# Optimization experiments

Hardware: AMD Instinct MI355X
Metric: run time of the kernel (lower is better)

Reference implementation:

```python
import jax, jax.numpy as jnp
import numpy as np

N = 262144        # total nodes in the batched graph
E = 8388608       # edges (avg degree 32)
DIM = 128         # gin_dimension
MAXDEG = 64       # max_node_deg + 1 (embedding table rows)
BN_EPS = 1e-5
SLOPE = 0.01      # leaky_relu default negative slope


def _batchnorm(x, gamma, beta):
    # training-mode BatchNorm1d: batch statistics over the node dimension
    mu = x.mean(axis=0)
    var = x.var(axis=0)
    return (x - mu) / jnp.sqrt(var + BN_EPS) * gamma + beta


def setup_inputs() -> dict:
    key = jax.random.key(0)
    ks = jax.random.split(key, 12)
    node_deg = jax.random.randint(ks[0], (N,), 0, MAXDEG)
    edge_index = jax.random.randint(ks[1], (2, E), 0, N)
    pos = jax.random.normal(ks[2], (N, 3), dtype=jnp.float32)
    # learned parameters
    embed_deg = jax.random.normal(ks[3], (MAXDEG, DIM), dtype=jnp.float32) * 0.02
    eps = jnp.zeros((), dtype=jnp.float32)  # GINConv train_eps, init 0
    W_conv = jax.random.normal(ks[4], (3, DIM), dtype=jnp.float32) * 0.5
    b_conv = jnp.full((DIM,), 0.01, dtype=jnp.float32)
    bn1_gamma = jnp.ones((DIM,), dtype=jnp.float32)
    bn1_beta = jnp.zeros((DIM,), dtype=jnp.float32)
    fc_W1 = jax.random.normal(ks[5], (2 * DIM, DIM), dtype=jnp.float32) * 0.06
    fc_b1 = jnp.full((DIM,), 0.01, dtype=jnp.float32)
    fc_bn_gamma = jnp.ones((DIM,), dtype=jnp.float32)
    fc_bn_beta = jnp.zeros((DIM,), dtype=jnp.float32)
    fc_W2 = jax.random.normal(ks[6], (DIM, 1), dtype=jnp.float32) * 0.12
    fc_b2 = jnp.full((1,), 0.01, dtype=jnp.float32)
    return {
        "node_deg": node_deg, "edge_index": edge_index, "pos": pos,
        "embed_deg": embed_deg, "eps": eps, "W_conv": W_conv, "b_conv": b_conv,
        "bn1_gamma": bn1_gamma, "bn1_beta": bn1_beta,
        "fc_W1": fc_W1, "fc_b1": fc_b1,
        "fc_bn_gamma": fc_bn_gamma, "fc_bn_beta": fc_bn_beta,
        "fc_W2": fc_W2, "fc_b2": fc_b2,
    }


def reference(node_deg, edge_index, pos, embed_deg, eps, W_conv, b_conv,
              bn1_gamma, bn1_beta, fc_W1, fc_b1, fc_bn_gamma, fc_bn_beta,
              fc_W2, fc_b2):
    src, dst = edge_index[0], edge_index[1]
    # GINConv (train_eps): mlp((1+eps)*x + sum_{j->i} x_j), mlp = Linear(3, DIM)
    agg = jax.ops.segment_sum(pos[src], dst, num_segments=N)  # [N, 3]
    x = ((1.0 + eps) * pos + agg) @ W_conv + b_conv            # [N, DIM]
    x = jax.nn.leaky_relu(_batchnorm(x, bn1_gamma, bn1_beta), SLOPE)
    # degree embedding branch
    tmp = embed_deg[node_deg]                                  # [N, DIM]
    xc = jnp.concatenate([tmp, x], axis=1)                     # [N, 2*DIM]
    # fc head: Linear -> BN -> LeakyReLU -> Linear -> Sigmoid -> squeeze
    h = xc @ fc_W1 + fc_b1
    h = jax.nn.leaky_relu(_batchnorm(h, fc_bn_gamma, fc_bn_beta), SLOPE)
    out = jax.nn.sigmoid(h @ fc_W2 + fc_b2)
    return out[:, 0]                                           # [N] node filtration values
```

## Files before the change

kernel.cpp:

```cpp
#include <hip/hip_runtime.h>

#define N_NODES 262144
#define N_EDGES 8388608
#define EPB 8192
#define NBLK (N_EDGES / EPB)
#define NBKT 1024

typedef unsigned int uint32;
typedef unsigned short ushort16;
typedef __attribute__((ext_vector_type(8))) short short8v;
typedef __attribute__((ext_vector_type(4))) float f32x4;

__device__ __forceinline__ float bf2f(uint32 u) { return __uint_as_float(u << 16); }
__device__ __forceinline__ ushort16 f2bf(float x) {
    uint32 u = __float_as_uint(x);
    u = (u + 0x7fffu + ((u >> 16) & 1u)) >> 16;
    return (ushort16)u;
}
__device__ __forceinline__ float lrelu(float v) { return v > 0.f ? v : 0.01f * v; }

__global__ __launch_bounds__(256) void k_hist(const int* __restrict__ ei,
                                              uint32* __restrict__ counts) {
    __shared__ uint32 cnt[NBKT];
    int t = threadIdx.x;
    for (int j = t; j < NBKT; j += 256) cnt[j] = 0;
    __syncthreads();
    int base = blockIdx.x * EPB;
    for (int ch = 0; ch < EPB / 256; ++ch) {
        int d = ei[N_EDGES + base + ch * 256 + t];
        atomicAdd(&cnt[d >> 8], 1u);
    }
    __syncthreads();
    for (int j = t; j < NBKT; j += 256) counts[blockIdx.x * NBKT + j] = cnt[j];
}

__global__ __launch_bounds__(256) void k_scanB(const uint32* __restrict__ counts,
                                               uint32* __restrict__ offsL,
                                               uint32* __restrict__ btot) {
    int b = blockIdx.x, t = threadIdx.x;
    uint32 a[4], s = 0;
    #pragma unroll
    for (int j = 0; j < 4; ++j) { a[j] = counts[(4 * t + j) * NBKT + b]; s += a[j]; }
    int lane = t & 63, wid = t >> 6;
    uint32 v = s;
    #pragma unroll
    for (int o = 1; o < 64; o <<= 1) {
        uint32 u = __shfl_up(v, o, 64);
        if (lane >= o) v += u;
    }
    __shared__ uint32 wt[4];
    if (lane == 63) wt[wid] = v;
    __syncthreads();
    uint32 wbase = 0;
    for (int w = 0; w < wid; ++w) wbase += wt[w];
    uint32 run = wbase + v - s;
    #pragma unroll
    for (int j = 0; j < 4; ++j) { offsL[(4 * t + j) * NBKT + b] = run; run += a[j]; }
    if (t == 255) btot[b] = run;
}

__global__ __launch_bounds__(256) void k_scanTot(const uint32* __restrict__ btot,
                                                 uint32* __restrict__ bstart) {
    int t = threadIdx.x;
    uint32 c[4], s = 0;
    #pragma unroll
    for (int j = 0; j < 4; ++j) { c[j] = btot[t * 4 + j]; s += c[j]; }
    int lane = t & 63, wid = t >> 6;
    uint32 v = s;
    #pragma unroll
    for (int o = 1; o < 64; o <<= 1) {
        uint32 u = __shfl_up(v, o, 64);
        if (lane >= o) v += u;
    }
    __shared__ uint32 wt[4];
    if (lane == 63) wt[wid] = v;
    __syncthreads();
    uint32 wbase = 0;
    for (int w = 0; w < wid; ++w) wbase += wt[w];
    uint32 run = wbase + v - s;
    #pragma unroll
    for (int j = 0; j < 4; ++j) { bstart[t * 4 + j] = run; run += c[j]; }
}

__global__ __launch_bounds__(256) void k_bin(const int* __restrict__ ei,
                                             const uint32* __restrict__ offsL,
                                             const uint32* __restrict__ bstart,
                                             uint32* __restrict__ binned) {
    __shared__ uint32 cnt[NBKT];
    __shared__ uint32 base[NBKT];
    int t = threadIdx.x;
    for (int j = t; j < NBKT; j += 256) {
        cnt[j] = 0;
        base[j] = bstart[j] + offsL[blockIdx.x * NBKT + j];
    }
    __syncthreads();
    int eb = blockIdx.x * EPB;
    for (int ch = 0; ch < EPB / 256; ++ch) {
        int e = eb + ch * 256 + t;
        uint32 s = (uint32)ei[e];
        uint32 d = (uint32)ei[N_EDGES + e];
        uint32 b = d >> 8;
        uint32 r = atomicAdd(&cnt[b], 1u);
        binned[base[b] + r] = (s << 8) | (d & 255u);
    }
}

__global__ __launch_bounds__(256) void k_accum(const uint32* __restrict__ binned,
                                               const uint32* __restrict__ bstart,
                                               const uint32* __restrict__ btot,
                                               const float* __restrict__ pos,
                                               float* __restrict__ agg) {
    __shared__ float acc[768];
    int t = threadIdx.x;
    acc[t] = 0.f; acc[256 + t] = 0.f; acc[512 + t] = 0.f;
    __syncthreads();
    int b = blockIdx.x;
    uint32 st = bstart[b], ct = btot[b];
    for (uint32 i = t; i < ct; i += 256) {
        uint32 w = binned[st + i];
        uint32 s = w >> 8, dl = w & 255u;
        const float* p = pos + 3 * s;
        float p0 = p[0], p1 = p[1], p2 = p[2];
        atomicAdd(&acc[dl * 3 + 0], p0);
        atomicAdd(&acc[dl * 3 + 1], p1);
        atomicAdd(&acc[dl * 3 + 2], p2);
    }
    __syncthreads();
    float* o = agg + (size_t)b * 768;
    o[t] = acc[t]; o[256 + t] = acc[256 + t]; o[512 + t] = acc[512 + t];
}

__global__ __launch_bounds__(256) void k_scatter(const int* __restrict__ ei,
                                                 const float* __restrict__ pos,
                                                 float* __restrict__ agg) {
    int e = blockIdx.x * 256 + threadIdx.x;
    int s = ei[e];
    int d = ei[N_EDGES + e];
    const float* p = pos + 3 * s;
    float* a = agg + 3 * d;
    atomicAdd(a + 0, p[0]);
    atomicAdd(a + 1, p[1]);
    atomicAdd(a + 2, p[2]);
}

__global__ __launch_bounds__(256) void k_y_moments(const float* __restrict__ pos,
                                                   const float* __restrict__ agg,
                                                   const float* __restrict__ epsp,
                                                   float* __restrict__ y,
                                                   float* __restrict__ mom) {
    int n = blockIdx.x * 256 + threadIdx.x;
    float e1 = 1.f + epsp[0];
    float y0 = e1 * pos[3 * n + 0] + agg[3 * n + 0];
    float y1 = e1 * pos[3 * n + 1] + agg[3 * n + 1];
    float y2 = e1 * pos[3 * n + 2] + agg[3 * n + 2];
    y[3 * n + 0] = y0; y[3 * n + 1] = y1; y[3 * n + 2] = y2;
    float m[9] = {y0, y1, y2, y0 * y0, y0 * y1, y0 * y2, y1 * y1, y1 * y2, y2 * y2};
    #pragma unroll
    for (int j = 0; j < 9; ++j) {
        #pragma unroll
        for (int o = 1; o < 64; o <<= 1) m[j] += __shfl_xor(m[j], o, 64);
    }
    __shared__ float buf[4][9];
    int lane = threadIdx.x & 63, wid = threadIdx.x >> 6;
    if (lane == 0) {
        #pragma unroll
        for (int j = 0; j < 9; ++j) buf[wid][j] = m[j];
    }
    __syncthreads();
    if (threadIdx.x < 9) {
        float s = buf[0][threadIdx.x] + buf[1][threadIdx.x] + buf[2][threadIdx.x] + buf[3][threadIdx.x];
        atomicAdd(&mom[threadIdx.x], s);
    }
}

__global__ __launch_bounds__(128) void k_bn1(const float* __restrict__ mom,
                                             const float* __restrict__ Wc,
                                             const float* __restrict__ bc,
                                             const float* __restrict__ g1,
                                             const float* __restrict__ be1,
                                             float* __restrict__ A3,
                                             float* __restrict__ cvec) {
    int d = threadIdx.x;
    float inv = 1.f / (float)N_NODES;
    float m0 = mom[0] * inv, m1 = mom[1] * inv, m2 = mom[2] * inv;
    float c00 = mom[3] * inv - m0 * m0;
    float c01 = mom[4] * inv - m0 * m1;
    float c02 = mom[5] * inv - m0 * m2;
    float c11 = mom[6] * inv - m1 * m1;
    float c12 = mom[7] * inv - m1 * m2;
    float c22 = mom[8] * inv - m2 * m2;
    float w0 = Wc[d], w1 = Wc[128 + d], w2 = Wc[256 + d];
    float mu = m0 * w0 + m1 * w1 + m2 * w2 + bc[d];
    float var = c00 * w0 * w0 + c11 * w1 * w1 + c22 * w2 * w2 +
                2.f * (c01 * w0 * w1 + c02 * w0 * w2 + c12 * w1 * w2);
    float s1 = g1[d] * rsqrtf(var + 1e-5f);
    float sh1 = be1[d] - mu * s1;
    A3[d] = w0 * s1;
    A3[128 + d] = w1 * s1;
    A3[256 + d] = w2 * s1;
    cvec[d] = bc[d] * s1 + sh1;
}

__global__ __launch_bounds__(128) void k_e64(const float* __restrict__ emb,
                                             const float* __restrict__ W1,
                                             const float* __restrict__ b1,
                                             float* __restrict__ E64b) {
    int c = blockIdx.x, d = threadIdx.x;
    float acc = b1[d];
    for (int k = 0; k < 128; ++k) acc += emb[c * 128 + k] * W1[k * 128 + d];
    E64b[c * 128 + d] = acc;
}

__global__ __launch_bounds__(256, 2) void k_gemm_mfma(const float* __restrict__ y,
                                                      const int* __restrict__ deg,
                                                      const float* __restrict__ A3,
                                                      const float* __restrict__ cvec,
                                                      const float* __restrict__ W1,
                                                      const float* __restrict__ E64b,
                                                      float* __restrict__ partial,
                                                      ushort16* __restrict__ hout) {
    __shared__ __align__(16) char Lraw[128 * 132 * 4];
    __shared__ float red[512];
    short* Wl = (short*)Lraw;
    short* Xl = (short*)(Lraw + 32768);
    float* H  = (float*)Lraw;

    const int t = threadIdx.x;
    const int nbase = blockIdx.x * 128;

    {
        int n = t & 127, kh = t >> 7;
        int nf = n >> 4, n16 = n & 15;
        #pragma unroll
        for (int q = 0; q < 8; ++q) {
            int kb = kh * 64 + q * 8;
            short pk[8];
            #pragma unroll
            for (int j = 0; j < 8; ++j)
                pk[j] = (short)f2bf(W1[(128 + kb + j) * 128 + n]);
            int s = kb >> 5, kg = (kb >> 3) & 3;
            *(short8v*)&Wl[(((nf * 4 + s) * 4 + kg) * 16 + n16) * 8] = *(short8v*)pk;
        }
    }
    {
        int k8 = t & 15, mg = t >> 4;
        f32x4 aA0 = *(const f32x4*)&A3[k8 * 8],       aA1 = *(const f32x4*)&A3[k8 * 8 + 4];
        f32x4 aB0 = *(const f32x4*)&A3[128 + k8 * 8], aB1 = *(const f32x4*)&A3[128 + k8 * 8 + 4];
        f32x4 aC0 = *(const f32x4*)&A3[256 + k8 * 8], aC1 = *(const f32x4*)&A3[256 + k8 * 8 + 4];
        f32x4 cv0 = *(const f32x4*)&cvec[k8 * 8],     cv1 = *(const f32x4*)&cvec[k8 * 8 + 4];
        int s = k8 >> 2, kg = k8 & 3;
        #pragma unroll
        for (int mm = 0; mm < 8; ++mm) {
            int m = mg * 8 + mm;
            const float* yy = y + (size_t)(nbase + m) * 3;
            float y0 = yy[0], y1 = yy[1], y2 = yy[2];
            short pk[8];
            #pragma unroll
            for (int j = 0; j < 4; ++j) {
                pk[j]     = (short)f2bf(lrelu(y0 * aA0[j] + y1 * aB0[j] + y2 * aC0[j] + cv0[j]));
                pk[4 + j] = (short)f2bf(lrelu(y0 * aA1[j] + y1 * aB1[j] + y2 * aC1[j] + cv1[j]));
            }
            *(short8v*)&Xl[(((m >> 4) * 4 + s) * 4 + kg) * 16 * 8 + (m & 15) * 8] = *(short8v*)pk;
        }
    }
    __syncthreads();

    const int w = t >> 6, l = t & 63;
    const int lk = l >> 4, l16 = l & 15;
    f32x4 acc[2][8];
    #pragma unroll
    for (int a = 0; a < 2; ++a)
        #pragma unroll
        for (int b = 0; b < 8; ++b) acc[a][b] = (f32x4)(0.f);
    #pragma unroll
    for (int s = 0; s < 4; ++s) {
        short8v af[2], bf[8];
        #pragma unroll
        for (int mf2 = 0; mf2 < 2; ++mf2) {
            int mf = w * 2 + mf2;
            af[mf2] = *(short8v*)&Xl[(((mf * 4 + s) * 4 + lk) * 16 + l16) * 8];
        }
        #pragma unroll
        for (int nf = 0; nf < 8; ++nf)
            bf[nf] = *(short8v*)&Wl[(((nf * 4 + s) * 4 + lk) * 16 + l16) * 8];
        #pragma unroll
        for (int mf2 = 0; mf2 < 2; ++mf2)
            #pragma unroll
            for (int nf = 0; nf < 8; ++nf)
                acc[mf2][nf] = __builtin_amdgcn_mfma_f32_16x16x32_bf16(af[mf2], bf[nf], acc[mf2][nf], 0, 0, 0);
    }
    __syncthreads();

    #pragma unroll
    for (int mf2 = 0; mf2 < 2; ++mf2) {
        int rbase = (w * 2 + mf2) * 16 + lk * 4;
        #pragma unroll
        for (int nf = 0; nf < 8; ++nf) {
            int c = nf * 16 + l16;
            #pragma unroll
            for (int r = 0; r < 4; ++r)
                H[(rbase + r) * 132 + c] = acc[mf2][nf][r];
        }
    }
    __syncthreads();

    {
        int m = t >> 1, ch = (t & 1) * 64;
        int node = nbase + m;
        int dg = deg[node];
        const float* Er = E64b + (size_t)dg * 128 + ch;
        #pragma unroll
        for (int q = 0; q < 8; ++q) {
            int c = ch + q * 8;
            f32x4 h0 = *(f32x4*)&H[m * 132 + c];
            f32x4 h1 = *(f32x4*)&H[m * 132 + c + 4];
            f32x4 e0 = *(const f32x4*)&Er[q * 8];
            f32x4 e1 = *(const f32x4*)&Er[q * 8 + 4];
            h0 += e0; h1 += e1;
            *(f32x4*)&H[m * 132 + c] = h0;
            *(f32x4*)&H[m * 132 + c + 4] = h1;
            uint32 pk[4];
            #pragma unroll
            for (int j = 0; j < 4; ++j) {
                float lo = (j < 2) ? h0[2 * j] : h1[2 * (j - 2)];
                float hi = (j < 2) ? h0[2 * j + 1] : h1[2 * (j - 2) + 1];
                pk[j] = (uint32)f2bf(lo) | ((uint32)f2bf(hi) << 16);
            }
            *(uint4*)&hout[(size_t)node * 128 + c] = *(uint4*)pk;
        }
    }
    __syncthreads();

    {
        int c2 = t & 127, nh = t >> 7;
        float ps = 0.f, pq = 0.f;
        #pragma unroll 8
        for (int i = 0; i < 64; ++i) {
            float v = H[(nh * 64 + i) * 132 + c2];
            ps += v; pq += v * v;
        }
        red[t] = ps; red[256 + t] = pq;
    }
    __syncthreads();
    if (t < 128) {
        float S = red[t] + red[t + 128];
        float Q = red[256 + t] + red[256 + t + 128];
        partial[(size_t)blockIdx.x * 256 + t] = S;
        partial[(size_t)blockIdx.x * 256 + 128 + t] = Q;
    }
}

__global__ __launch_bounds__(256) void k_red(const float* __restrict__ partial,
                                             float* __restrict__ stat2) {
    int t = threadIdx.x;
    float s = 0.f;
    int rb = blockIdx.x * 64;
    for (int r = 0; r < 64; ++r) s += partial[(size_t)(rb + r) * 256 + t];
    atomicAdd(&stat2[t], s);
}

template <int MODE>
__global__ __launch_bounds__(256, 2) void k_main(const float* __restrict__ y,
                                                 const int* __restrict__ deg,
                                                 const float* __restrict__ A3,
                                                 const float* __restrict__ cvec,
                                                 const float* __restrict__ W1,
                                                 const float* __restrict__ E64b,
                                                 float* __restrict__ stat2,
                                                 const float* __restrict__ sc2,
                                                 const float* __restrict__ sh2,
                                                 const float* __restrict__ W2,
                                                 const float* __restrict__ b2,
                                                 float* __restrict__ out) {
    __shared__ float Wl[128][128];
    __shared__ float xl[32][128];
    for (int i = threadIdx.x; i < 128 * 128; i += 256)
        Wl[i >> 7][i & 127] = W1[16384 + i];
    const int fg = threadIdx.x & 15;
    const int np = threadIdx.x >> 4;
    const int f0 = fg * 8;
    const int n0 = np * 2;
    const int fx = threadIdx.x & 127;
    const int nb = threadIdx.x >> 7;
    float a0 = A3[fx], a1 = A3[128 + fx], a2 = A3[256 + fx], cv = cvec[fx];
    float ssum[8] = {0}, ssq[8] = {0};
    float s2v[8], t2v[8], w2v[8], b2v = 0.f;
    if constexpr (MODE == 2) {
        *(float4*)&s2v[0] = *(const float4*)&sc2[f0];
        *(float4*)&s2v[4] = *(const float4*)&sc2[f0 + 4];
        *(float4*)&t2v[0] = *(const float4*)&sh2[f0];
        *(float4*)&t2v[4] = *(const float4*)&sh2[f0 + 4];
        *(float4*)&w2v[0] = *(const float4*)&W2[f0];
        *(float4*)&w2v[4] = *(const float4*)&W2[f0 + 4];
        b2v = b2[0];
    }
    for (int it = 0; it < 4; ++it) {
        int nbase = (blockIdx.x * 4 + it) * 32;
        __syncthreads();
        #pragma unroll
        for (int s = 0; s < 16; ++s) {
            int n = nb + s * 2;
            const float* yy = y + (nbase + n) * 3;
            float v = yy[0] * a0 + yy[1] * a1 + yy[2] * a2 + cv;
            xl[n][fx] = lrelu(v);
        }
        __syncthreads();
        float acc0[8] = {0}, acc1[8] = {0};
        for (int k4 = 0; k4 < 32; ++k4) {
            float xs0[4], xs1[4];
            *(float4*)xs0 = *(const float4*)&xl[n0][k4 * 4];
            *(float4*)xs1 = *(const float4*)&xl[n0 + 1][k4 * 4];
            #pragma unroll
            for (int kk = 0; kk < 4; ++kk) {
                float4 wA = *(const float4*)&Wl[k4 * 4 + kk][f0];
                float4 wB = *(const float4*)&Wl[k4 * 4 + kk][f0 + 4];
                float xa = xs0[kk], xb = xs1[kk];
                acc0[0] += xa * wA.x; acc0[1] += xa * wA.y; acc0[2] += xa * wA.z; acc0[3] += xa * wA.w;
                acc0[4] += xa * wB.x; acc0[5] += xa * wB.y; acc0[6] += xa * wB.z; acc0[7] += xa * wB.w;
                acc1[0] += xb * wA.x; acc1[1] += xb * wA.y; acc1[2] += xb * wA.z; acc1[3] += xb * wA.w;
                acc1[4] += xb * wB.x; acc1[5] += xb * wB.y; acc1[6] += xb * wB.z; acc1[7] += xb * wB.w;
            }
        }
        int nA = nbase + n0, nB = nA + 1;
        int dA = deg[nA], dB = deg[nB];
        float eA[8], eB[8], hA[8], hB[8];
        *(float4*)&eA[0] = *(const float4*)&E64b[dA * 128 + f0];
        *(float4*)&eA[4] = *(const float4*)&E64b[dA * 128 + f0 + 4];
        *(float4*)&eB[0] = *(const float4*)&E64b[dB * 128 + f0];
        *(float4*)&eB[4] = *(const float4*)&E64b[dB * 128 + f0 + 4];
        #pragma unroll
        for (int j = 0; j < 8; ++j) { hA[j] = acc0[j] + eA[j]; hB[j] = acc1[j] + eB[j]; }
        if constexpr (MODE == 1) {
            #pragma unroll
            for (int j = 0; j < 8; ++j) {
                ssum[j] += hA[j] + hB[j];
                ssq[j] += hA[j] * hA[j] + hB[j] * hB[j];
            }
        }
        if constexpr (MODE == 2) {
            float pA = 0.f, pB = 0.f;
            #pragma unroll
            for (int j = 0; j < 8; ++j) {
                pA += lrelu(hA[j] * s2v[j] + t2v[j]) * w2v[j];
                pB += lrelu(hB[j] * s2v[j] + t2v[j]) * w2v[j];
            }
            #pragma unroll
            for (int o = 1; o < 16; o <<= 1) {
                pA += __shfl_xor(pA, o, 64);
                pB += __shfl_xor(pB, o, 64);
            }
            if (fg == 0) {
                out[nA] = 1.f / (1.f + expf(-(pA + b2v)));
                out[nB] = 1.f / (1.f + expf(-(pB + b2v)));
            }
        }
    }
    if constexpr (MODE == 1) {
        __syncthreads();
        #pragma unroll
        for (int j = 0; j < 8; ++j) {
            ssum[j] += __shfl_xor(ssum[j], 16, 64);
            ssum[j] += __shfl_xor(ssum[j], 32, 64);
            ssq[j] += __shfl_xor(ssq[j], 16, 64);
            ssq[j] += __shfl_xor(ssq[j], 32, 64);
        }
        float* redp = &xl[0][0];
        int lane = threadIdx.x & 63, wid = threadIdx.x >> 6;
        if (lane < 16) {
            #pragma unroll
            for (int j = 0; j < 8; ++j) {
                redp[wid * 256 + lane * 16 + j] = ssum[j];
                redp[wid * 256 + lane * 16 + 8 + j] = ssq[j];
            }
        }
        __syncthreads();
        if (threadIdx.x < 128) {
            int d = threadIdx.x, fgg = d >> 3, j = d & 7;
            float s = redp[fgg * 16 + j] + redp[256 + fgg * 16 + j] +
                      redp[512 + fgg * 16 + j] + redp[768 + fgg * 16 + j];
            float q = redp[fgg * 16 + 8 + j] + redp[256 + fgg * 16 + 8 + j] +
                      redp[512 + fgg * 16 + 8 + j] + redp[768 + fgg * 16 + 8 + j];
            atomicAdd(&stat2[d], s);
            atomicAdd(&stat2[128 + d], q);
        }
    }
}

__global__ __launch_bounds__(128) void k_bn2(const float* __restrict__ stat2,
                                             const float* __restrict__ g2,
                                             const float* __restrict__ be2,
                                             float* __restrict__ sc2,
                                             float* __restrict__ sh2) {
    int d = threadIdx.x;
    float inv = 1.f / (float)N_NODES;
    float mu = stat2[d] * inv;
    float var = stat2[128 + d] * inv - mu * mu;
    float s = g2[d] * rsqrtf(var + 1e-5f);
    sc2[d] = s;
    sh2[d] = be2[d] - mu * s;
}

__global__ __launch_bounds__(256) void k_final_h(const ushort16* __restrict__ h,
                                                 const float* __restrict__ sc2,
                                                 const float* __restrict__ sh2,
                                                 const float* __restrict__ W2,
                                                 const float* __restrict__ b2,
                                                 float* __restrict__ out) {
    int t = blockIdx.x * 256 + threadIdx.x;
    int node = t >> 3, part = t & 7;
    const ushort16* hp = h + (size_t)node * 128 + part * 16;
    uint32 ua[4], ub[4];
    *(uint4*)ua = *(const uint4*)hp;
    *(uint4*)ub = *(const uint4*)(hp + 8);
    int fb = part * 16;
    float pd = 0.f;
    #pragma unroll
    for (int q = 0; q < 4; ++q) {
        int f = fb + 2 * q;
        float v0 = bf2f(ua[q] & 0xffffu), v1 = bf2f(ua[q] >> 16);
        pd += lrelu(v0 * sc2[f] + sh2[f]) * W2[f];
        pd += lrelu(v1 * sc2[f + 1] + sh2[f + 1]) * W2[f + 1];
        int g = fb + 8 + 2 * q;
        float w0 = bf2f(ub[q] & 0xffffu), w1 = bf2f(ub[q] >> 16);
        pd += lrelu(w0 * sc2[g] + sh2[g]) * W2[g];
        pd += lrelu(w1 * sc2[g + 1] + sh2[g + 1]) * W2[g + 1];
    }
    pd += __shfl_xor(pd, 1, 64);
    pd += __shfl_xor(pd, 2, 64);
    pd += __shfl_xor(pd, 4, 64);
    if (part == 0) out[node] = 1.f / (1.f + expf(-(pd + b2[0])));
}

extern "C" void kernel_launch(void* const* d_in, const int* in_sizes, int n_in,
                              void* d_out, int out_size, void* d_ws, size_t ws_size,
                              hipStream_t stream) {
    const int*   node_deg = (const int*)d_in[0];
    const int*   ei       = (const int*)d_in[1];
    const float* pos      = (const float*)d_in[2];
    const float* emb      = (const float*)d_in[3];
    const float* epsp     = (const float*)d_in[4];
    const float* Wc       = (const float*)d_in[5];
    const float* bc       = (const float*)d_in[6];
    const float* g1       = (const float*)d_in[7];
    const float* be1      = (const float*)d_in[8];
    const float* W1       = (const float*)d_in[9];
    const float* b1       = (const float*)d_in[10];
    const float* g2       = (const float*)d_in[11];
    const float* be2      = (const float*)d_in[12];
    const float* W2       = (const float*)d_in[13];
    const float* b2       = (const float*)d_in[14];
    float* out = (float*)d_out;

    float* F = (float*)d_ws;
    float* agg    = F;
    float* y      = F + 786432;
    float* mom    = F + 1572864;
    float* stat2  = F + 1572880;
    float* A3     = F + 1573136;
    float* cvec   = F + 1573520;
    float* E64b   = F + 1573648;
    float* sc2    = F + 1581840;
    float* sh2    = F + 1581968;
    uint32* bstart = (uint32*)(F + 1582096);
    uint32* btot   = (uint32*)(F + 1583120);
    float* U      = F + 1584144;
    uint32* binned = (uint32*)U;
    uint32* counts = (uint32*)(U + 8388608);
    uint32* offsL  = (uint32*)(U + 9437184);
    ushort16* hbuf = (ushort16*)U;
    float* partial = agg;

    const size_t needBinH  = (size_t)(1584144 + 16777216) * 4;
    const size_t needBin   = (size_t)(1584144 + 10485760) * 4;
    bool useBin, storeH;
    if      (ws_size >= needBinH) { useBin = true;  storeH = true;  }
    else if (ws_size >= needBin)  { useBin = true;  storeH = false; }
    else                          { useBin = false; storeH = false; }

    hipMemsetAsync(mom, 0, 272 * 4, stream);

    if (useBin) {
        k_hist<<<NBLK, 256, 0, stream>>>(ei, counts);
        k_scanB<<<NBKT, 256, 0, stream>>>(counts, offsL, btot);
        k_scanTot<<<1, 256, 0, stream>>>(btot, bstart);
        k_bin<<<NBLK, 256, 0, stream>>>(ei, offsL, bstart, binned);
        k_accum<<<NBKT, 256, 0, stream>>>(binned, bstart, btot, pos, agg);
    } else {
        hipMemsetAsync(agg, 0, 786432 * 4, stream);
        k_scatter<<<N_EDGES / 256, 256, 0, stream>>>(ei, pos, agg);
    }
    k_y_moments<<<N_NODES / 256, 256, 0, stream>>>(pos, agg, epsp, y, mom);
    k_bn1<<<1, 128, 0, stream>>>(mom, Wc, bc, g1, be1, A3, cvec);
    k_e64<<<64, 128, 0, stream>>>(emb, W1, b1, E64b);

    if (storeH) {
        k_gemm_mfma<<<N_NODES / 128, 256, 0, stream>>>(y, node_deg, A3, cvec, W1,
                                                       E64b, partial, hbuf);
        k_red<<<32, 256, 0, stream>>>(partial, stat2);
        k_bn2<<<1, 128, 0, stream>>>(stat2, g2, be2, sc2, sh2);
        k_final_h<<<N_NODES / 32, 256, 0, stream>>>(hbuf, sc2, sh2, W2, b2, out);
    } else {
        k_main<1><<<2048, 256, 0, stream>>>(y, node_deg, A3, cvec, W1, E64b, stat2,
                                            nullptr, nullptr, nullptr, nullptr, nullptr);
        k_bn2<<<1, 128, 0, stream>>>(stat2, g2, be2, sc2, sh2);
        k_main<2><<<2048, 256, 0, stream>>>(y, node_deg, A3, cvec, W1, E64b, stat2,
                                            sc2, sh2, W2, b2, out);
    }
}
```

Baseline: 519.1 us.

## Coarsen edge buckets, stage binning in LDS, split accumulation into partials

Buckets grow from 256 to 1024 destination nodes, which cuts the bucket count to 256 and simplifies the histogram and scan kernels. The binning kernel now sorts each block's edges locally in LDS before writing, so global stores to each bucket are contiguous rather than scattered. Accumulation splits each bucket across 4 blocks that write partial sums, and the moments kernel adds the 4 partials. This trades extra partial-sum traffic and more LDS per block for better write coalescing and more parallelism in accumulation.

```diff
diff --git a/kernel.cpp b/kernel.cpp
--- a/kernel.cpp
+++ b/kernel.cpp
@@ -4,10 +4,13 @@
 #define N_EDGES 8388608
 #define EPB 8192
 #define NBLK (N_EDGES / EPB)
-#define NBKT 1024
+#define NBKT 256
+#define BSH 10
+#define ACC_SPLIT 4
 
 typedef unsigned int uint32;
 typedef unsigned short ushort16;
+typedef unsigned char uchar8;
 typedef __attribute__((ext_vector_type(8))) short short8v;
 typedef __attribute__((ext_vector_type(4))) float f32x4;
 
@@ -23,15 +26,15 @@
                                               uint32* __restrict__ counts) {
     __shared__ uint32 cnt[NBKT];
     int t = threadIdx.x;
-    for (int j = t; j < NBKT; j += 256) cnt[j] = 0;
+    cnt[t] = 0;
     __syncthreads();
     int base = blockIdx.x * EPB;
     for (int ch = 0; ch < EPB / 256; ++ch) {
         int d = ei[N_EDGES + base + ch * 256 + t];
-        atomicAdd(&cnt[d >> 8], 1u);
-    }
-    __syncthreads();
-    for (int j = t; j < NBKT; j += 256) counts[blockIdx.x * NBKT + j] = cnt[j];
+        atomicAdd(&cnt[d >> BSH], 1u);
+    }
+    __syncthreads();
+    counts[blockIdx.x * NBKT + t] = cnt[t];
 }
 
 __global__ __launch_bounds__(256) void k_scanB(const uint32* __restrict__ counts,
@@ -62,46 +65,75 @@
 __global__ __launch_bounds__(256) void k_scanTot(const uint32* __restrict__ btot,
                                                  uint32* __restrict__ bstart) {
     int t = threadIdx.x;
-    uint32 c[4], s = 0;
-    #pragma unroll
-    for (int j = 0; j < 4; ++j) { c[j] = btot[t * 4 + j]; s += c[j]; }
+    uint32 v = btot[t];
+    uint32 inc = v;
     int lane = t & 63, wid = t >> 6;
-    uint32 v = s;
     #pragma unroll
     for (int o = 1; o < 64; o <<= 1) {
-        uint32 u = __shfl_up(v, o, 64);
-        if (lane >= o) v += u;
+        uint32 u = __shfl_up(inc, o, 64);
+        if (lane >= o) inc += u;
     }
     __shared__ uint32 wt[4];
-    if (lane == 63) wt[wid] = v;
+    if (lane == 63) wt[wid] = inc;
     __syncthreads();
     uint32 wbase = 0;
     for (int w = 0; w < wid; ++w) wbase += wt[w];
-    uint32 run = wbase + v - s;
-    #pragma unroll
-    for (int j = 0; j < 4; ++j) { bstart[t * 4 + j] = run; run += c[j]; }
+    bstart[t] = wbase + inc - v;
 }
 
 __global__ __launch_bounds__(256) void k_bin(const int* __restrict__ ei,
                                              const uint32* __restrict__ offsL,
                                              const uint32* __restrict__ bstart,
                                              uint32* __restrict__ binned) {
+    __shared__ uint32 pay[EPB];
+    __shared__ uchar8 bkt[EPB];
     __shared__ uint32 cnt[NBKT];
-    __shared__ uint32 base[NBKT];
+    __shared__ uint32 lstart[NBKT];
+    __shared__ uint32 cursor[NBKT];
+    __shared__ uint32 gbase[NBKT];
+    __shared__ uint32 wt[4];
     int t = threadIdx.x;
-    for (int j = t; j < NBKT; j += 256) {
-        cnt[j] = 0;
-        base[j] = bstart[j] + offsL[blockIdx.x * NBKT + j];
-    }
+    cnt[t] = 0;
+    gbase[t] = bstart[t] + offsL[blockIdx.x * NBKT + t];
     __syncthreads();
     int eb = blockIdx.x * EPB;
+    for (int ch = 0; ch < EPB / 256; ++ch) {
+        int d = ei[N_EDGES + eb + ch * 256 + t];
+        atomicAdd(&cnt[d >> BSH], 1u);
+    }
+    __syncthreads();
+    {
+        uint32 v = cnt[t];
+        uint32 inc = v;
+        int lane = t & 63, wid = t >> 6;
+        #pragma unroll
+        for (int o = 1; o < 64; o <<= 1) {
+            uint32 u = __shfl_up(inc, o, 64);
+            if (lane >= o) inc += u;
+        }
+        if (lane == 63) wt[wid] = inc;
+        __syncthreads();
+        uint32 wbase = 0;
+        for (int w = 0; w < wid; ++w) wbase += wt[w];
+        uint32 ex = wbase + inc - v;
+        lstart[t] = ex;
+        cursor[t] = ex;
+    }
+    __syncthreads();
     for (int ch = 0; ch < EPB / 256; ++ch) {
         int e = eb + ch * 256 + t;
         uint32 s = (uint32)ei[e];
         uint32 d = (uint32)ei[N_EDGES + e];
-        uint32 b = d >> 8;
-        uint32 r = atomicAdd(&cnt[b], 1u);
-        binned[base[b] + r] = (s << 8) | (d & 255u);
+        uint32 b = d >> BSH;
+        uint32 p = atomicAdd(&cursor[b], 1u);
+        pay[p] = (s << BSH) | (d & ((1u << BSH) - 1u));
+        bkt[p] = (uchar8)b;
+    }
+    __syncthreads();
+    for (int ch = 0; ch < EPB / 256; ++ch) {
+        int p = ch * 256 + t;
+        uint32 b = bkt[p];
+        binned[gbase[b] + (uint32)p - lstart[b]] = pay[p];
     }
 }
 
@@ -109,16 +141,19 @@
                                                const uint32* __restrict__ bstart,
                                                const uint32* __restrict__ btot,
                                                const float* __restrict__ pos,
-                                               float* __restrict__ agg) {
-    __shared__ float acc[768];
+                                               float* __restrict__ partialAgg) {
+    __shared__ float acc[3072];
     int t = threadIdx.x;
-    acc[t] = 0.f; acc[256 + t] = 0.f; acc[512 + t] = 0.f;
-    __syncthreads();
-    int b = blockIdx.x;
+    for (int i = t; i < 3072; i += 256) acc[i] = 0.f;
+    __syncthreads();
+    int b = blockIdx.x >> 2;
+    int q = blockIdx.x & 3;
     uint32 st = bstart[b], ct = btot[b];
-    for (uint32 i = t; i < ct; i += 256) {
-        uint32 w = binned[st + i];
-        uint32 s = w >> 8, dl = w & 255u;
+    uint32 lo = st + (uint32)(((unsigned long long)ct * q) >> 2);
+    uint32 hi = st + (uint32)(((unsigned long long)ct * (q + 1)) >> 2);
+    for (uint32 i = lo + t; i < hi; i += 256) {
+        uint32 w = binned[i];
+        uint32 s = w >> BSH, dl = w & ((1u << BSH) - 1u);
         const float* p = pos + 3 * s;
         float p0 = p[0], p1 = p[1], p2 = p[2];
         atomicAdd(&acc[dl * 3 + 0], p0);
@@ -126,8 +161,8 @@
         atomicAdd(&acc[dl * 3 + 2], p2);
     }
     __syncthreads();
-    float* o = agg + (size_t)b * 768;
-    o[t] = acc[t]; o[256 + t] = acc[256 + t]; o[512 + t] = acc[512 + t];
+    float* o = partialAgg + (size_t)blockIdx.x * 3072;
+    for (int i = t; i < 3072; i += 256) o[i] = acc[i];
 }
 
 __global__ __launch_bounds__(256) void k_scatter(const int* __restrict__ ei,
@@ -143,16 +178,30 @@
     atomicAdd(a + 2, p[2]);
 }
 
+template <int R>
 __global__ __launch_bounds__(256) void k_y_moments(const float* __restrict__ pos,
-                                                   const float* __restrict__ agg,
+                                                   const float* __restrict__ aggP,
                                                    const float* __restrict__ epsp,
                                                    float* __restrict__ y,
                                                    float* __restrict__ mom) {
     int n = blockIdx.x * 256 + threadIdx.x;
     float e1 = 1.f + epsp[0];
-    float y0 = e1 * pos[3 * n + 0] + agg[3 * n + 0];
-    float y1 = e1 * pos[3 * n + 1] + agg[3 * n + 1];
-    float y2 = e1 * pos[3 * n + 2] + agg[3 * n + 2];
+    float a0, a1, a2;
+    if constexpr (R == 4) {
+        size_t base = (size_t)(n >> BSH) * 4 * 3072 + (size_t)(n & ((1 << BSH) - 1)) * 3;
+        a0 = a1 = a2 = 0.f;
+        #pragma unroll
+        for (int q = 0; q < 4; ++q) {
+            a0 += aggP[base + (size_t)q * 3072 + 0];
+            a1 += aggP[base + (size_t)q * 3072 + 1];
+            a2 += aggP[base + (size_t)q * 3072 + 2];
+        }
+    } else {
+        a0 = aggP[3 * n + 0]; a1 = aggP[3 * n + 1]; a2 = aggP[3 * n + 2];
+    }
+    float y0 = e1 * pos[3 * n + 0] + a0;
+    float y1 = e1 * pos[3 * n + 1] + a1;
+    float y2 = e1 * pos[3 * n + 2] + a2;
     y[3 * n + 0] = y0; y[3 * n + 1] = y1; y[3 * n + 2] = y2;
     float m[9] = {y0, y1, y2, y0 * y0, y0 * y1, y0 * y2, y1 * y1, y1 * y2, y2 * y2};
     #pragma unroll
@@ -564,14 +613,15 @@
     uint32* bstart = (uint32*)(F + 1582096);
     uint32* btot   = (uint32*)(F + 1583120);
     float* U      = F + 1584144;
-    uint32* binned = (uint32*)U;
-    uint32* counts = (uint32*)(U + 8388608);
-    uint32* offsL  = (uint32*)(U + 9437184);
-    ushort16* hbuf = (ushort16*)U;
+    uint32* binned   = (uint32*)U;
+    uint32* counts   = (uint32*)(U + 8388608);
+    uint32* offsL    = (uint32*)(U + 8650752);
+    float*  partialA = U + 8912896;
+    ushort16* hbuf   = (ushort16*)U;
     float* partial = agg;
 
     const size_t needBinH  = (size_t)(1584144 + 16777216) * 4;
-    const size_t needBin   = (size_t)(1584144 + 10485760) * 4;
+    const size_t needBin   = (size_t)(1584144 + 12058624) * 4;
     bool useBin, storeH;
     if      (ws_size >= needBinH) { useBin = true;  storeH = true;  }
     else if (ws_size >= needBin)  { useBin = true;  storeH = false; }
@@ -584,12 +634,13 @@
         k_scanB<<<NBKT, 256, 0, stream>>>(counts, offsL, btot);
         k_scanTot<<<1, 256, 0, stream>>>(btot, bstart);
         k_bin<<<NBLK, 256, 0, stream>>>(ei, offsL, bstart, binned);
-        k_accum<<<NBKT, 256, 0, stream>>>(binned, bstart, btot, pos, agg);
+        k_accum<<<NBKT * ACC_SPLIT, 256, 0, stream>>>(binned, bstart, btot, pos, partialA);
+        k_y_moments<4><<<N_NODES / 256, 256, 0, stream>>>(pos, partialA, epsp, y, mom);
     } else {
         hipMemsetAsync(agg, 0, 786432 * 4, stream);
         k_scatter<<<N_EDGES / 256, 256, 0, stream>>>(ei, pos, agg);
-    }
-    k_y_moments<<<N_NODES / 256, 256, 0, stream>>>(pos, agg, epsp, y, mom);
+        k_y_moments<1><<<N_NODES / 256, 256, 0, stream>>>(pos, agg, epsp, y, mom);
+    }
     k_bn1<<<1, 128, 0, stream>>>(mom, Wc, bc, g1, be1, A3, cvec);
     k_e64<<<64, 128, 0, stream>>>(emb, W1, b1, E64b);
 
```

Result: faster. 431.4 us (-16.9%).
